# Optimization experiments

Hardware: AMD Instinct MI355X
Metric: run time of the kernel (lower is better)

Reference implementation:

```python
import jax, jax.numpy as jnp
import numpy as np

TEMPERATURE = 0.07
IGNORE_INDEX = 255
MAX_SAMPLES = 1024  # K
BACKGROUND = 0
EPS = 1e-8


def setup_inputs() -> dict:
    key = jax.random.key(0)
    k1, k2 = jax.random.split(key)
    B, C, H, W = 16, 256, 128, 128
    feats = jax.random.normal(k1, (B, C, H, W), dtype=jnp.float32)
    labels = jax.random.randint(k2, (B, H, W), 0, 4).astype(jnp.int64)
    return {"feats": feats, "labels": labels}


def _sample_pixels(feats_flat, labels_flat, K):
    """Deterministic analogue of the torch sampler: positives first, then
    background negatives, invalid last (original uses randperm; the math
    downstream is identical for any such selection). Pads exactly like the
    original: zero features, ignore_index labels, boolean valid mask."""
    # priority: 0 = foreground pos, 1 = background neg, 2 = ignore
    prio = jnp.where(labels_flat == IGNORE_INDEX, 2,
                     jnp.where(labels_flat == BACKGROUND, 1, 0))
    order = jnp.argsort(prio, axis=1)[:, :K]                      # [B, K] stable sort
    sel_prio = jnp.take_along_axis(prio, order, axis=1)
    valid = sel_prio < 2                                          # [B, K] bool
    s_feats = jnp.take_along_axis(feats_flat, order[:, :, None], axis=1)
    s_feats = s_feats * valid[:, :, None].astype(s_feats.dtype)   # zero-pad like F.pad
    s_labels = jnp.where(valid, jnp.take_along_axis(labels_flat, order, axis=1),
                         IGNORE_INDEX)
    return s_feats, s_labels, valid


def reference(feats, labels):
    B, C, H, W = feats.shape
    K = MAX_SAMPLES
    f = feats.transpose(0, 2, 3, 1).reshape(B, H * W, C)          # [B, N, C]
    l = labels.reshape(B, H * W)

    s_feats, s_labels, valid = _sample_pixels(f, l, K)

    # pair each image with the next (rolled) image -> [B, 2K, .]
    fp = jnp.concatenate([s_feats, jnp.roll(s_feats, -1, axis=0)], axis=1)
    lp = jnp.concatenate([s_labels, jnp.roll(s_labels, -1, axis=0)], axis=1)
    vp = jnp.concatenate([valid, jnp.roll(valid, -1, axis=0)], axis=1)

    # F.normalize(dim=2), eps=1e-12
    fp = fp / jnp.maximum(jnp.linalg.norm(fp, axis=2, keepdims=True), 1e-12)

    vf = vp.astype(fp.dtype)
    logits = jnp.einsum('bkc,bjc->bkj', fp, fp) / TEMPERATURE      # [B, 2K, 2K]
    logits = logits - jax.lax.stop_gradient(jnp.max(logits, axis=2, keepdims=True))

    v_matrix = vf[:, :, None] * vf[:, None, :]
    pos_mask = (lp[:, :, None] == lp[:, None, :]).astype(fp.dtype) * v_matrix
    same_img = jnp.kron(jnp.eye(2, dtype=fp.dtype), jnp.ones((K, K), dtype=fp.dtype))[None]
    neg_mask = (1.0 - pos_mask) * same_img * v_matrix
    not_self = 1.0 - jnp.eye(2 * K, dtype=fp.dtype)[None]
    pos_mask = pos_mask * not_self
    neg_mask = neg_mask * not_self

    exp_logits = jnp.exp(logits)
    sum_neg = jnp.sum(exp_logits * neg_mask, axis=2, keepdims=True)
    log_probs = logits - jnp.log(exp_logits + sum_neg + EPS)

    num_pos = jnp.maximum(pos_mask.sum(axis=2), 1.0)
    mean_log_prob = (pos_mask * log_probs).sum(axis=2) / num_pos
    valid_anchors = (pos_mask.sum(axis=2) > 0).astype(fp.dtype)
    loss_img = (-mean_log_prob * valid_anchors).sum(axis=1) / jnp.maximum(
        valid_anchors.sum(axis=1), 1.0)                            # [B]

    # with valid labels everywhere, every chunk is valid -> divide by B
    return loss_img.sum() / B
```

## Files before the change

### kernel.cpp

```cpp
#include <hip/hip_runtime.h>
#include <hip/hip_bf16.h>

namespace {

constexpr int NB  = 16;
constexpr int NC  = 256;
constexpr int NHW = 16384;
constexpr int NK  = 1024;
constexpr int IGN = 255;
constexpr float SCALE = 4.5398164f;
constexpr float CBIAS = 20.609929f;
constexpr float LN2   = 0.69314718f;

typedef __attribute__((ext_vector_type(8))) short short8;
typedef __attribute__((ext_vector_type(4))) float f32x4;
typedef unsigned int u32;

#define ASM_VMCNT8 asm volatile("s_waitcnt vmcnt(8)" ::: "memory")
#define ASM_VMCNT0 asm volatile("s_waitcnt vmcnt(0)" ::: "memory")
#define ASM_LGKM0  asm volatile("s_waitcnt lgkmcnt(0)" ::: "memory")
#define SCHEDB     __builtin_amdgcn_sched_barrier(0)
#define MEMFENCE   asm volatile("" ::: "memory")
#define BARRIER    __builtin_amdgcn_s_barrier()

__device__ __forceinline__ float fexp2(float x) {
#if __has_builtin(__builtin_amdgcn_exp2f)
  return __builtin_amdgcn_exp2f(x);
#else
  return exp2f(x);
#endif
}

__device__ __forceinline__ void gl_lds16(const void* g, void* l) {
  __builtin_amdgcn_global_load_lds((const __attribute__((address_space(1))) u32*)g,
                                   (__attribute__((address_space(3))) u32*)l, 16, 0, 0);
}

__global__ __launch_bounds__(256) void pcl_sample(const int* __restrict__ labels,
                                                  int* __restrict__ sel_lab,
                                                  int* __restrict__ sel_idx,
                                                  int* __restrict__ counter) {
  const int b = blockIdx.x, t = threadIdx.x, lane = t & 63, w = t >> 6;
  if (b == 0 && t == 0) counter[0] = 0;
  __shared__ int labL[NHW];
  __shared__ int wtot[4];

  for (int k = t; k < NK; k += 256) {
    sel_lab[b * NK + k] = IGN;
    sel_idx[b * NK + k] = 0;
  }

  const int* lab = labels + b * NHW;
  for (int k = 0; k < 64; ++k) {
    int idx = k * 256 + t;
    int pos = (idx & ~63) | ((idx & 63) ^ ((idx >> 6) & 31));
    labL[pos] = lab[idx];
  }
  __syncthreads();

  const int base = t * 64, m5 = t & 31;
  int cfg = 0, cbg = 0;
  for (int i = 0; i < 64; ++i) {
    int L = labL[base + (i ^ m5)];
    cfg += (L != IGN && L != 0);
    cbg += (L == 0);
  }
  int packed = cfg | (cbg << 15);
  int incl = packed;
#pragma unroll
  for (int off = 1; off < 64; off <<= 1) {
    int n = __shfl_up(incl, off);
    if (lane >= off) incl += n;
  }
  if (lane == 63) wtot[w] = incl;
  __syncthreads();
  int wb = 0, total = 0;
  for (int ww = 0; ww < 4; ++ww) { int v = wtot[ww]; total += v; if (ww < w) wb += v; }
  int excl = incl - packed + wb;
  int rf  = excl & 32767;
  int rbg = (excl >> 15) & 32767;
  const int nfg = total & 32767;
  if (rf < NK || nfg + rbg < NK) {
    for (int i = 0; i < 64; ++i) {
      int L = labL[base + (i ^ m5)];
      if (L == IGN) continue;
      if (L != 0) {
        if (rf < NK) { sel_lab[b * NK + rf] = L; sel_idx[b * NK + rf] = base + i; }
        ++rf;
      } else {
        int s = nfg + rbg;
        if (s < NK) { sel_lab[b * NK + s] = L; sel_idx[b * NK + s] = base + i; }
        ++rbg;
      }
    }
  }
}

__global__ __launch_bounds__(1024) void pcl_gather(const float* __restrict__ feats,
                                                   const int* __restrict__ sel_lab,
                                                   const int* __restrict__ sel_idx,
                                                   unsigned short* __restrict__ SF) {
  const int b = blockIdx.x >> 4, kb = blockIdx.x & 15;
  const int t = threadIdx.x, s = t & 63, w = t >> 6;
  __shared__ float fbuf[64][257];
  __shared__ float sqs[16][64];
  __shared__ float rn[64];
  const int gk = b * NK + kb * 64 + s;
  const int lb = sel_lab[gk];
  const int p = (lb != IGN) ? sel_idx[gk] : -1;
  const float* fb = feats + (size_t)b * NC * NHW;
  float sq = 0.f;
#pragma unroll
  for (int cc = 0; cc < 16; ++cc) {
    int c = w * 16 + cc;
    float v = (p >= 0) ? fb[(size_t)c * NHW + p] : 0.f;
    fbuf[s][c] = v;
    sq += v * v;
  }
  sqs[w][s] = sq;
  __syncthreads();
  if (t < 64) {
    float tot = 0.f;
#pragma unroll
    for (int k2 = 0; k2 < 16; ++k2) tot += sqs[k2][t];
    rn[t] = SCALE / fmaxf(sqrtf(tot), 1e-12f);
  }
  __syncthreads();
#pragma unroll
  for (int it = 0; it < 2; ++it) {
    int slot = it * 1024 + t;
    int ss = slot >> 5, ch = slot & 31;
    float r = rn[ss];
    short8 v8;
#pragma unroll
    for (int e = 0; e < 8; ++e) {
      float x = fbuf[ss][ch * 8 + e] * r;
      __hip_bfloat16 h = __float2bfloat16(x);
      unsigned short u; __builtin_memcpy(&u, &h, 2);
      v8[e] = (short)u;
    }
    *(short8*)(SF + ((size_t)(b * NK + kb * 64 + ss)) * NC + ch * 8) = v8;
  }
}

__global__ __launch_bounds__(512) void pcl_tiles(
    const unsigned short* __restrict__ SF, const int* __restrict__ sel_lab,
    float2* __restrict__ SNd, float4* __restrict__ Rii, float4* __restrict__ Rin,
    float4* __restrict__ Cp) {
  const int id = blockIdx.x;
  const int i = id & 15, strip = id >> 4, inxt = (i + 1) & 15;
  const int t = threadIdx.x, lane = t & 63, w = t >> 6;
  const int rw = w & 3, ch2 = w >> 2;
  const int lg = lane >> 4, lr = lane & 15;

  __shared__ short buf[2][128 * 256];
  __shared__ float4 colAcc[4][128];
  __shared__ float4 rred[2][64];

  const unsigned short* SFrow = SF + (size_t)i * (NK * NC) + strip * 64 * NC;

  auto stage_round = [&](int rr) {
    const unsigned short* base =
        SF + (size_t)((rr < 8) ? i : inxt) * (NK * NC) + ((rr & 7) * 128) * NC;
    short* dst = buf[rr & 1];
#pragma unroll
    for (int it = 0; it < 8; ++it) {
      int n = it * 512 + t, row = n >> 5, ch = n & 31;
      gl_lds16(base + row * NC + ((ch ^ (row & 15)) << 3), dst + (size_t)n * 8);
    }
  };

#pragma unroll
  for (int it = 0; it < 4; ++it) {
    int n = it * 512 + t, row = n >> 5, ch = n & 31;
    gl_lds16(SFrow + row * NC + ((ch ^ (row & 15)) << 3), buf[0] + (size_t)n * 8);
  }
  ASM_VMCNT0; MEMFENCE; BARRIER; MEMFENCE;

  short8 afrag[8];
  const int arow = rw * 16 + lr;
#pragma unroll
  for (int ks = 0; ks < 8; ++ks) {
    int ch = ks * 4 + lg;
    afrag[ks] = *(const short8*)(buf[0] + arow * 256 + ((ch ^ (arow & 15)) << 3));
  }
  ASM_LGKM0; SCHEDB; MEMFENCE; BARRIER; MEMFENCE;

  stage_round(0);
  stage_round(1);

  int rlab[4];
#pragma unroll
  for (int jj = 0; jj < 4; ++jj) {
    int L = sel_lab[i * NK + strip * 64 + rw * 16 + 4 * lg + jj];
    rlab[jj] = (L == IGN) ? -1 : L;
  }

  ASM_VMCNT8; MEMFENCE; BARRIER; MEMFENCE;

  float S1[4], NP[4], PE[4], SNL[4];
#pragma unroll
  for (int jj = 0; jj < 4; ++jj) { S1[jj] = 0.f; NP[jj] = 0.f; PE[jj] = 0.f; SNL[jj] = 0.f; }

  for (int r = 0; r < 8; ++r) {
    int cl[4];
#pragma unroll
    for (int c2 = 0; c2 < 4; ++c2)
      cl[c2] = sel_lab[i * NK + r * 128 + ch2 * 64 + c2 * 16 + lr];

    const short* bbase = buf[r & 1];
    f32x4 acc[4];
#pragma unroll
    for (int c2 = 0; c2 < 4; ++c2) acc[c2] = f32x4{0.f, 0.f, 0.f, 0.f};
#pragma unroll
    for (int ks = 0; ks < 8; ++ks) {
      int ch = ks * 4 + lg;
      short8 af = afrag[ks];
#pragma unroll
      for (int c2 = 0; c2 < 4; ++c2) {
        int brow = ch2 * 64 + c2 * 16 + lr;
        short8 bf = *(const short8*)(bbase + brow * 256 + ((ch ^ (brow & 15)) << 3));
        acc[c2] = __builtin_amdgcn_mfma_f32_16x16x32_bf16(af, bf, acc[c2], 0, 0, 0);
      }
    }

    const int grb = strip * 64 + rw * 16 + 4 * lg;
#pragma unroll
    for (int c2 = 0; c2 < 4; ++c2) {
      const bool cv = (cl[c2] != IGN);
      const int gc = r * 128 + ch2 * 64 + c2 * 16 + lr;
#pragma unroll
      for (int jj = 0; jj < 4; ++jj) {
        float y = acc[c2][jj] - CBIAS;
        float E = fexp2(y);
        bool pos = cv && (rlab[jj] == cl[c2]) && (grb + jj != gc);
        bool neg = cv && (rlab[jj] != cl[c2]);
        float pm = pos ? 1.f : 0.f;
        S1[jj] += pm * y; NP[jj] += pm; PE[jj] += pm * E;
        SNL[jj] += neg ? E : 0.f;
      }
    }

    MEMFENCE; BARRIER; MEMFENCE;
    stage_round(r + 2);
    ASM_VMCNT8;
    MEMFENCE; BARRIER; MEMFENCE;
  }

#pragma unroll
  for (int jj = 0; jj < 4; ++jj) {
    float a = S1[jj], b4 = NP[jj], c4 = PE[jj], d4 = SNL[jj];
#pragma unroll
    for (int m = 1; m <= 8; m <<= 1) {
      a += __shfl_xor(a, m); b4 += __shfl_xor(b4, m);
      c4 += __shfl_xor(c4, m); d4 += __shfl_xor(d4, m);
    }
    if (lr == 4 * lg + jj) rred[ch2][rw * 16 + 4 * lg + jj] = make_float4(a, b4, c4, d4);
  }
  ASM_LGKM0; SCHEDB; MEMFENCE; BARRIER; MEMFENCE;
  if (ch2 == 0) {
#pragma unroll
    for (int jj = 0; jj < 4; ++jj) {
      if (lr == 4 * lg + jj) {
        int row = rw * 16 + 4 * lg + jj;
        float4 A4 = rred[0][row], B4 = rred[1][row];
        float sn = A4.w + B4.w + 1e-8f;
        int g = i * NK + strip * 64 + row;
        SNd[g] = make_float2(__logf(sn), 1.f / sn);
        Rii[g] = make_float4(A4.x + B4.x, A4.y + B4.y, A4.z + B4.z, 0.f);
      }
    }
  }
#pragma unroll
  for (int jj = 0; jj < 4; ++jj) { S1[jj] = 0.f; NP[jj] = 0.f; PE[jj] = 0.f; }

  for (int r = 8; r < 16; ++r) {
    int cl[4];
#pragma unroll
    for (int c2 = 0; c2 < 4; ++c2)
      cl[c2] = sel_lab[inxt * NK + (r & 7) * 128 + ch2 * 64 + c2 * 16 + lr];

    const short* bbase = buf[r & 1];
    f32x4 acc[4];
#pragma unroll
    for (int c2 = 0; c2 < 4; ++c2) acc[c2] = f32x4{0.f, 0.f, 0.f, 0.f};
#pragma unroll
    for (int ks = 0; ks < 8; ++ks) {
      int ch = ks * 4 + lg;
      short8 af = afrag[ks];
#pragma unroll
      for (int c2 = 0; c2 < 4; ++c2) {
        int brow = ch2 * 64 + c2 * 16 + lr;
        short8 bf = *(const short8*)(bbase + brow * 256 + ((ch ^ (brow & 15)) << 3));
        acc[c2] = __builtin_amdgcn_mfma_f32_16x16x32_bf16(af, bf, acc[c2], 0, 0, 0);
      }
    }

#pragma unroll
    for (int c2 = 0; c2 < 4; ++c2) {
      const bool cv = (cl[c2] != IGN);
      float cS = 0.f, cN = 0.f, cE = 0.f;
#pragma unroll
      for (int jj = 0; jj < 4; ++jj) {
        float y = acc[c2][jj] - CBIAS;
        float E = fexp2(y);
        float pm = (cv && (rlab[jj] == cl[c2])) ? 1.f : 0.f;
        S1[jj] += pm * y; NP[jj] += pm; PE[jj] += pm * E;
        cS += pm * y; cN += pm; cE += pm * E;
      }
      cS += __shfl_xor(cS, 16); cS += __shfl_xor(cS, 32);
      cN += __shfl_xor(cN, 16); cN += __shfl_xor(cN, 32);
      cE += __shfl_xor(cE, 16); cE += __shfl_xor(cE, 32);
      if (lg == 0) colAcc[rw][ch2 * 64 + c2 * 16 + lr] = make_float4(cS, cN, cE, 0.f);
    }
    ASM_LGKM0; SCHEDB;
    MEMFENCE; BARRIER; MEMFENCE;
    if (rw == 0) {
      int col = ch2 * 64 + lane;
      float4 A4 = colAcc[0][col], B4 = colAcc[1][col];
      float4 C4 = colAcc[2][col], D4 = colAcc[3][col];
      Cp[(i * 16 + strip) * NK + (r & 7) * 128 + col] =
          make_float4(A4.x + B4.x + C4.x + D4.x, A4.y + B4.y + C4.y + D4.y,
                      A4.z + B4.z + C4.z + D4.z, 0.f);
    }
    if (r < 14) { stage_round(r + 2); ASM_VMCNT8; }
    else if (r == 14) { ASM_VMCNT0; }
    if (r < 15) { MEMFENCE; BARRIER; MEMFENCE; }
  }

#pragma unroll
  for (int jj = 0; jj < 4; ++jj) {
    float a = S1[jj], b4 = NP[jj], c4 = PE[jj];
#pragma unroll
    for (int m = 1; m <= 8; m <<= 1) {
      a += __shfl_xor(a, m); b4 += __shfl_xor(b4, m); c4 += __shfl_xor(c4, m);
    }
    if (lr == 4 * lg + jj) rred[ch2][rw * 16 + 4 * lg + jj] = make_float4(a, b4, c4, 0.f);
  }
  ASM_LGKM0; SCHEDB; MEMFENCE; BARRIER; MEMFENCE;
  if (ch2 == 0) {
#pragma unroll
    for (int jj = 0; jj < 4; ++jj) {
      if (lr == 4 * lg + jj) {
        int row = rw * 16 + 4 * lg + jj;
        float4 A4 = rred[0][row], B4 = rred[1][row];
        Rin[i * NK + strip * 64 + row] =
            make_float4(A4.x + B4.x, A4.y + B4.y, A4.z + B4.z, 0.f);
      }
    }
  }
}

__global__ __launch_bounds__(1024) void pcl_assemble(const float4* __restrict__ Rii,
                                                     const float4* __restrict__ Rin,
                                                     const float4* __restrict__ Cp,
                                                     const float2* __restrict__ SNd,
                                                     float* __restrict__ Aimg,
                                                     int* __restrict__ counter,
                                                     float* __restrict__ out) {
  const int i = blockIdx.x, t = threadIdx.x, lane = t & 63, w = t >> 6;
  const int prev = (i + 15) & 15;
  const int r = t;
  float a1n = 0.f, a1c = 0.f, a2n = 0.f, a2c = 0.f;
  {
    float4 rii = Rii[i * NK + r];
    float4 rin = Rin[i * NK + r];
    float2 sn = SNd[i * NK + r];
    float pp_ii = LN2 * rii.x - rii.y * sn.x - sn.y * rii.z;
    float pp_in = LN2 * rin.x - rin.y * sn.x - sn.y * rin.z;
    float np1 = rii.y + rin.y;
    if (np1 > 0.f) { a1n = -(pp_ii + pp_in) / np1; a1c = 1.f; }
    float cs1 = 0.f, cnp = 0.f, cpe = 0.f;
#pragma unroll
    for (int s2 = 0; s2 < 16; ++s2) {
      float4 c = Cp[(prev * 16 + s2) * NK + r];
      cs1 += c.x; cnp += c.y; cpe += c.z;
    }
    float ppc = LN2 * cs1 - cnp * sn.x - sn.y * cpe;
    float np2 = rii.y + cnp;
    if (np2 > 0.f) { a2n = -(pp_ii + ppc) / np2; a2c = 1.f; }
  }
#pragma unroll
  for (int m = 1; m <= 32; m <<= 1) {
    a1n += __shfl_xor(a1n, m); a1c += __shfl_xor(a1c, m);
    a2n += __shfl_xor(a2n, m); a2c += __shfl_xor(a2c, m);
  }
  __shared__ float wred[16][4];
  __shared__ int lastf;
  if (lane == 0) { wred[w][0] = a1n; wred[w][1] = a1c; wred[w][2] = a2n; wred[w][3] = a2c; }
  __syncthreads();
  if (t == 0) {
    float s0 = 0.f, s1 = 0.f, s2 = 0.f, s3 = 0.f;
#pragma unroll
    for (int k2 = 0; k2 < 16; ++k2) {
      s0 += wred[k2][0]; s1 += wred[k2][1]; s2 += wred[k2][2]; s3 += wred[k2][3];
    }
    Aimg[i * 4 + 0] = s0; Aimg[i * 4 + 1] = s1;
    Aimg[i * 4 + 2] = s2; Aimg[i * 4 + 3] = s3;
    __threadfence();
    int old = atomicAdd(counter, 1);
    lastf = (old == NB - 1);
  }
  __syncthreads();
  if (lastf && t < 64) {
    float v = 0.f;
    if (t < NB) {
      int nb = (t + 1) & 15;
      float num = __hip_atomic_load(&Aimg[t * 4 + 0], __ATOMIC_ACQUIRE, __HIP_MEMORY_SCOPE_AGENT)
                + __hip_atomic_load(&Aimg[nb * 4 + 2], __ATOMIC_ACQUIRE, __HIP_MEMORY_SCOPE_AGENT);
      float cnt = __hip_atomic_load(&Aimg[t * 4 + 1], __ATOMIC_ACQUIRE, __HIP_MEMORY_SCOPE_AGENT)
                + __hip_atomic_load(&Aimg[nb * 4 + 3], __ATOMIC_ACQUIRE, __HIP_MEMORY_SCOPE_AGENT);
      v = num / fmaxf(cnt, 1.f);
    }
    v += __shfl_xor(v, 1); v += __shfl_xor(v, 2); v += __shfl_xor(v, 4); v += __shfl_xor(v, 8);
    if (t == 0) out[0] = v / (float)NB;
  }
}

}

extern "C" void kernel_launch(void* const* d_in, const int* in_sizes, int n_in,
                              void* d_out, int out_size, void* d_ws, size_t ws_size,
                              hipStream_t stream) {
  (void)in_sizes; (void)n_in; (void)out_size; (void)ws_size;
  const float* feats  = (const float*)d_in[0];
  const int*   labels = (const int*)d_in[1];
  float* out = (float*)d_out;
  char* ws = (char*)d_ws;

  int* sel_lab = (int*)ws;
  int* sel_idx = (int*)(ws + (64 << 10));
  unsigned short* SF = (unsigned short*)(ws + (128 << 10));
  size_t off = (128 << 10) + (size_t)NB * NK * NC * 2;
  float2* SNd = (float2*)(ws + off);  off += (size_t)NB * NK * 8;
  float4* Rii = (float4*)(ws + off);  off += (size_t)NB * NK * 16;
  float4* Rin = (float4*)(ws + off);  off += (size_t)NB * NK * 16;
  float4* Cp  = (float4*)(ws + off);  off += (size_t)NB * 16 * NK * 16;
  float* Aimg = (float*)(ws + off);   off += 64 * sizeof(float);
  int* counter = (int*)(ws + off);

  pcl_sample<<<NB, 256, 0, stream>>>(labels, sel_lab, sel_idx, counter);
  pcl_gather<<<256, 1024, 0, stream>>>(feats, sel_lab, sel_idx, SF);
  pcl_tiles<<<256, 512, 0, stream>>>(SF, sel_lab, SNd, Rii, Rin, Cp);
  pcl_assemble<<<NB, 1024, 0, stream>>>(Rii, Rin, Cp, SNd, Aimg, counter, out);
}
```

Baseline: 92.40 us.

## Fuse assemble stage into tiles kernel and retile MFMA to 2x2 per wave

The final assembly kernel is folded into the tiles kernel. Per-image atomic counters let the last finishing block of each image pair do the cross-strip reduction and write the final loss, which removes one launch and the Rin buffer. Each wave now computes a 2x2 grid of 16x16 MFMA tiles, so A and B fragments are reused. The bias subtraction is moved out of the exp loop and applied algebraically afterwards via a scale factor. The sampling kernel moves to 1024 threads with a padded LDS layout. The cost is a serialized tail in the last blocks and more registers per wave.

Measured after the change: 87.61 us. 5.2% less time.

```diff
diff --git a/kernel.cpp b/kernel.cpp
--- a/kernel.cpp
+++ b/kernel.cpp
@@ -22,46 +22,39 @@
 #define SCHEDB     __builtin_amdgcn_sched_barrier(0)
 #define MEMFENCE   asm volatile("" ::: "memory")
 #define BARRIER    __builtin_amdgcn_s_barrier()
-
-__device__ __forceinline__ float fexp2(float x) {
-#if __has_builtin(__builtin_amdgcn_exp2f)
-  return __builtin_amdgcn_exp2f(x);
-#else
-  return exp2f(x);
-#endif
-}
+#define ACQ_AGENT  __builtin_amdgcn_fence(__ATOMIC_ACQUIRE, "agent")
+
+__device__ __forceinline__ float fexp2(float x) { return __builtin_exp2f(x); }
 
 __device__ __forceinline__ void gl_lds16(const void* g, void* l) {
   __builtin_amdgcn_global_load_lds((const __attribute__((address_space(1))) u32*)g,
                                    (__attribute__((address_space(3))) u32*)l, 16, 0, 0);
 }
 
-__global__ __launch_bounds__(256) void pcl_sample(const int* __restrict__ labels,
-                                                  int* __restrict__ sel_lab,
-                                                  int* __restrict__ sel_idx,
-                                                  int* __restrict__ counter) {
+__global__ __launch_bounds__(1024) void pcl_sample(const int* __restrict__ labels,
+                                                   int* __restrict__ sel_lab,
+                                                   int* __restrict__ sel_idx,
+                                                   int* __restrict__ cnt,
+                                                   int* __restrict__ findone) {
   const int b = blockIdx.x, t = threadIdx.x, lane = t & 63, w = t >> 6;
-  if (b == 0 && t == 0) counter[0] = 0;
-  __shared__ int labL[NHW];
-  __shared__ int wtot[4];
-
-  for (int k = t; k < NK; k += 256) {
-    sel_lab[b * NK + k] = IGN;
-    sel_idx[b * NK + k] = 0;
-  }
+  if (t == 0) { cnt[b] = 0; if (b == 0) *findone = 0; }
+  __shared__ int labL[1024 * 17];
+  __shared__ int wtot[16];
+
+  sel_lab[b * NK + t] = IGN;
 
   const int* lab = labels + b * NHW;
-  for (int k = 0; k < 64; ++k) {
-    int idx = k * 256 + t;
-    int pos = (idx & ~63) | ((idx & 63) ^ ((idx >> 6) & 31));
-    labL[pos] = lab[idx];
-  }
-  __syncthreads();
-
-  const int base = t * 64, m5 = t & 31;
+#pragma unroll
+  for (int k = 0; k < 16; ++k) {
+    int idx = k * 1024 + t;
+    labL[(idx >> 4) * 17 + (idx & 15)] = lab[idx];
+  }
+  __syncthreads();
+
   int cfg = 0, cbg = 0;
-  for (int i = 0; i < 64; ++i) {
-    int L = labL[base + (i ^ m5)];
+#pragma unroll
+  for (int i = 0; i < 16; ++i) {
+    int L = labL[t * 17 + i];
     cfg += (L != IGN && L != 0);
     cbg += (L == 0);
   }
@@ -75,21 +68,23 @@
   if (lane == 63) wtot[w] = incl;
   __syncthreads();
   int wb = 0, total = 0;
-  for (int ww = 0; ww < 4; ++ww) { int v = wtot[ww]; total += v; if (ww < w) wb += v; }
+#pragma unroll
+  for (int ww = 0; ww < 16; ++ww) { int v = wtot[ww]; total += v; if (ww < w) wb += v; }
   int excl = incl - packed + wb;
   int rf  = excl & 32767;
   int rbg = (excl >> 15) & 32767;
   const int nfg = total & 32767;
   if (rf < NK || nfg + rbg < NK) {
-    for (int i = 0; i < 64; ++i) {
-      int L = labL[base + (i ^ m5)];
+#pragma unroll
+    for (int i = 0; i < 16; ++i) {
+      int L = labL[t * 17 + i];
       if (L == IGN) continue;
       if (L != 0) {
-        if (rf < NK) { sel_lab[b * NK + rf] = L; sel_idx[b * NK + rf] = base + i; }
+        if (rf < NK) { sel_lab[b * NK + rf] = L; sel_idx[b * NK + rf] = t * 16 + i; }
         ++rf;
       } else {
         int s = nfg + rbg;
-        if (s < NK) { sel_lab[b * NK + s] = L; sel_idx[b * NK + s] = base + i; }
+        if (s < NK) { sel_lab[b * NK + s] = L; sel_idx[b * NK + s] = t * 16 + i; }
         ++rbg;
       }
     }
@@ -145,17 +140,23 @@
 
 __global__ __launch_bounds__(512) void pcl_tiles(
     const unsigned short* __restrict__ SF, const int* __restrict__ sel_lab,
-    float2* __restrict__ SNd, float4* __restrict__ Rii, float4* __restrict__ Rin,
-    float4* __restrict__ Cp) {
+    float2* __restrict__ SNd, float4* __restrict__ Rii, float4* __restrict__ Cp,
+    float2* __restrict__ A1arr, float2* __restrict__ Aimg,
+    int* __restrict__ cnt, int* __restrict__ findone, float* __restrict__ out) {
   const int id = blockIdx.x;
-  const int i = id & 15, strip = id >> 4, inxt = (i + 1) & 15;
+  const int i = id & 15, strip = id >> 4;
+  const int inxt = (i + 1) & 15, iprev = (i + 15) & 15;
   const int t = threadIdx.x, lane = t & 63, w = t >> 6;
-  const int rw = w & 3, ch2 = w >> 2;
+  const int rw = w & 1, ch4 = w >> 1;
   const int lg = lane >> 4, lr = lane & 15;
+  const float SFAC = __builtin_exp2f(-CBIAS);
 
   __shared__ short buf[2][128 * 256];
-  __shared__ float4 colAcc[4][128];
-  __shared__ float4 rred[2][64];
+  __shared__ float4 colAcc[2][128];
+  __shared__ float4 rredS[4][64];
+  __shared__ float4 rredX[4][64];
+  __shared__ float2 fold2[8];
+  __shared__ int fA, fB;
 
   const unsigned short* SFrow = SF + (size_t)i * (NK * NC) + strip * 64 * NC;
 
@@ -177,69 +178,94 @@
   }
   ASM_VMCNT0; MEMFENCE; BARRIER; MEMFENCE;
 
-  short8 afrag[8];
-  const int arow = rw * 16 + lr;
-#pragma unroll
-  for (int ks = 0; ks < 8; ++ks) {
-    int ch = ks * 4 + lg;
-    afrag[ks] = *(const short8*)(buf[0] + arow * 256 + ((ch ^ (arow & 15)) << 3));
+  short8 afrag[2][8];
+#pragma unroll
+  for (int rt = 0; rt < 2; ++rt) {
+    const int arow = rw * 32 + rt * 16 + lr;
+#pragma unroll
+    for (int ks = 0; ks < 8; ++ks) {
+      int ch = ks * 4 + lg;
+      afrag[rt][ks] = *(const short8*)(buf[0] + arow * 256 + ((ch ^ (arow & 15)) << 3));
+    }
   }
   ASM_LGKM0; SCHEDB; MEMFENCE; BARRIER; MEMFENCE;
 
   stage_round(0);
   stage_round(1);
 
-  int rlab[4];
-#pragma unroll
-  for (int jj = 0; jj < 4; ++jj) {
-    int L = sel_lab[i * NK + strip * 64 + rw * 16 + 4 * lg + jj];
-    rlab[jj] = (L == IGN) ? -1 : L;
-  }
+  int rlab[2][4];
+#pragma unroll
+  for (int rt = 0; rt < 2; ++rt)
+#pragma unroll
+    for (int jj = 0; jj < 4; ++jj) {
+      int L = sel_lab[i * NK + strip * 64 + rw * 32 + rt * 16 + 4 * lg + jj];
+      rlab[rt][jj] = (L == IGN) ? -1 : L;
+    }
 
   ASM_VMCNT8; MEMFENCE; BARRIER; MEMFENCE;
 
-  float S1[4], NP[4], PE[4], SNL[4];
-#pragma unroll
-  for (int jj = 0; jj < 4; ++jj) { S1[jj] = 0.f; NP[jj] = 0.f; PE[jj] = 0.f; SNL[jj] = 0.f; }
+  float SA[2][4], NPr[2][4], PEr[2][4], ETr[2][4];
+#pragma unroll
+  for (int rt = 0; rt < 2; ++rt)
+#pragma unroll
+    for (int jj = 0; jj < 4; ++jj) { SA[rt][jj] = 0.f; NPr[rt][jj] = 0.f; PEr[rt][jj] = 0.f; ETr[rt][jj] = 0.f; }
+
+  const int rs = strip >> 1;
+  const bool dwave = ((ch4 >> 1) == (strip & 1));
 
   for (int r = 0; r < 8; ++r) {
-    int cl[4];
-#pragma unroll
-    for (int c2 = 0; c2 < 4; ++c2)
-      cl[c2] = sel_lab[i * NK + r * 128 + ch2 * 64 + c2 * 16 + lr];
-
-    const short* bbase = buf[r & 1];
-    f32x4 acc[4];
-#pragma unroll
-    for (int c2 = 0; c2 < 4; ++c2) acc[c2] = f32x4{0.f, 0.f, 0.f, 0.f};
+    int cl[2]; float cvf[2];
+#pragma unroll
+    for (int c2 = 0; c2 < 2; ++c2) {
+      int L = sel_lab[i * NK + r * 128 + ch4 * 32 + c2 * 16 + lr];
+      cl[c2] = (L == IGN) ? -2 : L;
+      cvf[c2] = (L == IGN) ? 0.f : 1.f;
+    }
+
+    const short* bb = buf[r & 1];
+    f32x4 acc[2][2];
+#pragma unroll
+    for (int rt = 0; rt < 2; ++rt)
+#pragma unroll
+      for (int c2 = 0; c2 < 2; ++c2) acc[rt][c2] = f32x4{0.f, 0.f, 0.f, 0.f};
 #pragma unroll
     for (int ks = 0; ks < 8; ++ks) {
       int ch = ks * 4 + lg;
-      short8 af = afrag[ks];
-#pragma unroll
-      for (int c2 = 0; c2 < 4; ++c2) {
-        int brow = ch2 * 64 + c2 * 16 + lr;
-        short8 bf = *(const short8*)(bbase + brow * 256 + ((ch ^ (brow & 15)) << 3));
-        acc[c2] = __builtin_amdgcn_mfma_f32_16x16x32_bf16(af, bf, acc[c2], 0, 0, 0);
-      }
-    }
-
-    const int grb = strip * 64 + rw * 16 + 4 * lg;
-#pragma unroll
-    for (int c2 = 0; c2 < 4; ++c2) {
-      const bool cv = (cl[c2] != IGN);
-      const int gc = r * 128 + ch2 * 64 + c2 * 16 + lr;
-#pragma unroll
-      for (int jj = 0; jj < 4; ++jj) {
-        float y = acc[c2][jj] - CBIAS;
-        float E = fexp2(y);
-        bool pos = cv && (rlab[jj] == cl[c2]) && (grb + jj != gc);
-        bool neg = cv && (rlab[jj] != cl[c2]);
-        float pm = pos ? 1.f : 0.f;
-        S1[jj] += pm * y; NP[jj] += pm; PE[jj] += pm * E;
-        SNL[jj] += neg ? E : 0.f;
-      }
-    }
+      short8 b0, b1;
+      {
+        int br0 = ch4 * 32 + lr, br1 = ch4 * 32 + 16 + lr;
+        b0 = *(const short8*)(bb + br0 * 256 + ((ch ^ (br0 & 15)) << 3));
+        b1 = *(const short8*)(bb + br1 * 256 + ((ch ^ (br1 & 15)) << 3));
+      }
+      acc[0][0] = __builtin_amdgcn_mfma_f32_16x16x32_bf16(afrag[0][ks], b0, acc[0][0], 0, 0, 0);
+      acc[0][1] = __builtin_amdgcn_mfma_f32_16x16x32_bf16(afrag[0][ks], b1, acc[0][1], 0, 0, 0);
+      acc[1][0] = __builtin_amdgcn_mfma_f32_16x16x32_bf16(afrag[1][ks], b0, acc[1][0], 0, 0, 0);
+      acc[1][1] = __builtin_amdgcn_mfma_f32_16x16x32_bf16(afrag[1][ks], b1, acc[1][1], 0, 0, 0);
+    }
+
+    const bool isdiag = (r == rs) && dwave;
+#pragma unroll
+    for (int rt = 0; rt < 2; ++rt)
+#pragma unroll
+      for (int c2 = 0; c2 < 2; ++c2) {
+        const int clc = cl[c2]; const float cvc = cvf[c2];
+        const int gc = r * 128 + ch4 * 32 + c2 * 16 + lr;
+        const int grb = strip * 64 + rw * 32 + rt * 16 + 4 * lg;
+#pragma unroll
+        for (int jj = 0; jj < 4; ++jj) {
+          float a = acc[rt][c2][jj];
+          float E = fexp2(a);
+          float Ev = cvc * E;
+          float pm = (rlab[rt][jj] == clc) ? 1.f : 0.f;
+          if (isdiag) {
+            bool ok = (grb + jj) != gc;
+            pm = ok ? pm : 0.f;
+            Ev = ok ? Ev : 0.f;
+          }
+          SA[rt][jj] += pm * a; NPr[rt][jj] += pm;
+          PEr[rt][jj] += pm * Ev; ETr[rt][jj] += Ev;
+        }
+      }
 
     MEMFENCE; BARRIER; MEMFENCE;
     stage_round(r + 2);
@@ -248,173 +274,190 @@
   }
 
 #pragma unroll
-  for (int jj = 0; jj < 4; ++jj) {
-    float a = S1[jj], b4 = NP[jj], c4 = PE[jj], d4 = SNL[jj];
-#pragma unroll
-    for (int m = 1; m <= 8; m <<= 1) {
-      a += __shfl_xor(a, m); b4 += __shfl_xor(b4, m);
-      c4 += __shfl_xor(c4, m); d4 += __shfl_xor(d4, m);
-    }
-    if (lr == 4 * lg + jj) rred[ch2][rw * 16 + 4 * lg + jj] = make_float4(a, b4, c4, d4);
-  }
-  ASM_LGKM0; SCHEDB; MEMFENCE; BARRIER; MEMFENCE;
-  if (ch2 == 0) {
+  for (int rt = 0; rt < 2; ++rt)
 #pragma unroll
     for (int jj = 0; jj < 4; ++jj) {
-      if (lr == 4 * lg + jj) {
-        int row = rw * 16 + 4 * lg + jj;
-        float4 A4 = rred[0][row], B4 = rred[1][row];
-        float sn = A4.w + B4.w + 1e-8f;
-        int g = i * NK + strip * 64 + row;
-        SNd[g] = make_float2(__logf(sn), 1.f / sn);
-        Rii[g] = make_float4(A4.x + B4.x, A4.y + B4.y, A4.z + B4.z, 0.f);
-      }
-    }
-  }
-#pragma unroll
-  for (int jj = 0; jj < 4; ++jj) { S1[jj] = 0.f; NP[jj] = 0.f; PE[jj] = 0.f; }
+      float a = SA[rt][jj], b4 = NPr[rt][jj], c4 = PEr[rt][jj], d4 = ETr[rt][jj];
+#pragma unroll
+      for (int m = 1; m <= 8; m <<= 1) {
+        a += __shfl_xor(a, m); b4 += __shfl_xor(b4, m);
+        c4 += __shfl_xor(c4, m); d4 += __shfl_xor(d4, m);
+      }
+      if (lr == 0) rredS[ch4][rw * 32 + rt * 16 + 4 * lg + jj] = make_float4(a, b4, c4, d4);
+    }
+
+  float SX[2][4], NX[2][4], PX[2][4];
+#pragma unroll
+  for (int rt = 0; rt < 2; ++rt)
+#pragma unroll
+    for (int jj = 0; jj < 4; ++jj) { SX[rt][jj] = 0.f; NX[rt][jj] = 0.f; PX[rt][jj] = 0.f; }
 
   for (int r = 8; r < 16; ++r) {
-    int cl[4];
-#pragma unroll
-    for (int c2 = 0; c2 < 4; ++c2)
-      cl[c2] = sel_lab[inxt * NK + (r & 7) * 128 + ch2 * 64 + c2 * 16 + lr];
-
-    const short* bbase = buf[r & 1];
-    f32x4 acc[4];
-#pragma unroll
-    for (int c2 = 0; c2 < 4; ++c2) acc[c2] = f32x4{0.f, 0.f, 0.f, 0.f};
+    int cl[2];
+#pragma unroll
+    for (int c2 = 0; c2 < 2; ++c2) {
+      int L = sel_lab[inxt * NK + (r & 7) * 128 + ch4 * 32 + c2 * 16 + lr];
+      cl[c2] = (L == IGN) ? -2 : L;
+    }
+
+    const short* bb = buf[r & 1];
+    f32x4 acc[2][2];
+#pragma unroll
+    for (int rt = 0; rt < 2; ++rt)
+#pragma unroll
+      for (int c2 = 0; c2 < 2; ++c2) acc[rt][c2] = f32x4{0.f, 0.f, 0.f, 0.f};
 #pragma unroll
     for (int ks = 0; ks < 8; ++ks) {
       int ch = ks * 4 + lg;
-      short8 af = afrag[ks];
-#pragma unroll
-      for (int c2 = 0; c2 < 4; ++c2) {
-        int brow = ch2 * 64 + c2 * 16 + lr;
-        short8 bf = *(const short8*)(bbase + brow * 256 + ((ch ^ (brow & 15)) << 3));
-        acc[c2] = __builtin_amdgcn_mfma_f32_16x16x32_bf16(af, bf, acc[c2], 0, 0, 0);
-      }
-    }
-
-#pragma unroll
-    for (int c2 = 0; c2 < 4; ++c2) {
-      const bool cv = (cl[c2] != IGN);
-      float cS = 0.f, cN = 0.f, cE = 0.f;
-#pragma unroll
-      for (int jj = 0; jj < 4; ++jj) {
-        float y = acc[c2][jj] - CBIAS;
-        float E = fexp2(y);
-        float pm = (cv && (rlab[jj] == cl[c2])) ? 1.f : 0.f;
-        S1[jj] += pm * y; NP[jj] += pm; PE[jj] += pm * E;
-        cS += pm * y; cN += pm; cE += pm * E;
-      }
-      cS += __shfl_xor(cS, 16); cS += __shfl_xor(cS, 32);
-      cN += __shfl_xor(cN, 16); cN += __shfl_xor(cN, 32);
-      cE += __shfl_xor(cE, 16); cE += __shfl_xor(cE, 32);
-      if (lg == 0) colAcc[rw][ch2 * 64 + c2 * 16 + lr] = make_float4(cS, cN, cE, 0.f);
+      short8 b0, b1;
+      {
+        int br0 = ch4 * 32 + lr, br1 = ch4 * 32 + 16 + lr;
+        b0 = *(const short8*)(bb + br0 * 256 + ((ch ^ (br0 & 15)) << 3));
+        b1 = *(const short8*)(bb + br1 * 256 + ((ch ^ (br1 & 15)) << 3));
+      }
+      acc[0][0] = __builtin_amdgcn_mfma_f32_16x16x32_bf16(afrag[0][ks], b0, acc[0][0], 0, 0, 0);
+      acc[0][1] = __builtin_amdgcn_mfma_f32_16x16x32_bf16(afrag[0][ks], b1, acc[0][1], 0, 0, 0);
+      acc[1][0] = __builtin_amdgcn_mfma_f32_16x16x32_bf16(afrag[1][ks], b0, acc[1][0], 0, 0, 0);
+      acc[1][1] = __builtin_amdgcn_mfma_f32_16x16x32_bf16(afrag[1][ks], b1, acc[1][1], 0, 0, 0);
+    }
+
+    float cS[2], cN[2], cE[2];
+#pragma unroll
+    for (int c2 = 0; c2 < 2; ++c2) { cS[c2] = 0.f; cN[c2] = 0.f; cE[c2] = 0.f; }
+#pragma unroll
+    for (int rt = 0; rt < 2; ++rt)
+#pragma unroll
+      for (int c2 = 0; c2 < 2; ++c2) {
+        const int clc = cl[c2];
+#pragma unroll
+        for (int jj = 0; jj < 4; ++jj) {
+          float a = acc[rt][c2][jj];
+          float E = fexp2(a);
+          float pm = (rlab[rt][jj] == clc) ? 1.f : 0.f;
+          float pa = pm * a, pe = pm * E;
+          SX[rt][jj] += pa; NX[rt][jj] += pm; PX[rt][jj] += pe;
+          cS[c2] += pa; cN[c2] += pm; cE[c2] += pe;
+        }
+      }
+#pragma unroll
+    for (int c2 = 0; c2 < 2; ++c2) {
+      cS[c2] += __shfl_xor(cS[c2], 16); cS[c2] += __shfl_xor(cS[c2], 32);
+      cN[c2] += __shfl_xor(cN[c2], 16); cN[c2] += __shfl_xor(cN[c2], 32);
+      cE[c2] += __shfl_xor(cE[c2], 16); cE[c2] += __shfl_xor(cE[c2], 32);
+      if (lg == 0) colAcc[rw][ch4 * 32 + c2 * 16 + lr] = make_float4(cS[c2], cN[c2], cE[c2], 0.f);
     }
     ASM_LGKM0; SCHEDB;
     MEMFENCE; BARRIER; MEMFENCE;
-    if (rw == 0) {
-      int col = ch2 * 64 + lane;
-      float4 A4 = colAcc[0][col], B4 = colAcc[1][col];
-      float4 C4 = colAcc[2][col], D4 = colAcc[3][col];
-      Cp[(i * 16 + strip) * NK + (r & 7) * 128 + col] =
-          make_float4(A4.x + B4.x + C4.x + D4.x, A4.y + B4.y + C4.y + D4.y,
-                      A4.z + B4.z + C4.z + D4.z, 0.f);
-    }
-    if (r < 14) { stage_round(r + 2); ASM_VMCNT8; }
-    else if (r == 14) { ASM_VMCNT0; }
-    if (r < 15) { MEMFENCE; BARRIER; MEMFENCE; }
-  }
-
-#pragma unroll
-  for (int jj = 0; jj < 4; ++jj) {
-    float a = S1[jj], b4 = NP[jj], c4 = PE[jj];
-#pragma unroll
-    for (int m = 1; m <= 8; m <<= 1) {
-      a += __shfl_xor(a, m); b4 += __shfl_xor(b4, m); c4 += __shfl_xor(c4, m);
-    }
-    if (lr == 4 * lg + jj) rred[ch2][rw * 16 + 4 * lg + jj] = make_float4(a, b4, c4, 0.f);
-  }
-  ASM_LGKM0; SCHEDB; MEMFENCE; BARRIER; MEMFENCE;
-  if (ch2 == 0) {
+    if (rw == 1 && lg == 0) {
+#pragma unroll
+      for (int c2 = 0; c2 < 2; ++c2) {
+        int col = ch4 * 32 + c2 * 16 + lr;
+        float4 o = colAcc[0][col];
+        Cp[(i * 16 + strip) * NK + (r & 7) * 128 + col] =
+            make_float4(cS[c2] + o.x, cN[c2] + o.y, (cE[c2] + o.z) * SFAC, 0.f);
+      }
+    }
+    if (r < 14) { stage_round(r + 2); ASM_VMCNT8; MEMFENCE; BARRIER; MEMFENCE; }
+    else if (r == 14) { ASM_VMCNT0; MEMFENCE; BARRIER; MEMFENCE; }
+  }
+
+#pragma unroll
+  for (int rt = 0; rt < 2; ++rt)
 #pragma unroll
     for (int jj = 0; jj < 4; ++jj) {
-      if (lr == 4 * lg + jj) {
-        int row = rw * 16 + 4 * lg + jj;
-        float4 A4 = rred[0][row], B4 = rred[1][row];
-        Rin[i * NK + strip * 64 + row] =
-            make_float4(A4.x + B4.x, A4.y + B4.y, A4.z + B4.z, 0.f);
-      }
-    }
-  }
-}
-
-__global__ __launch_bounds__(1024) void pcl_assemble(const float4* __restrict__ Rii,
-                                                     const float4* __restrict__ Rin,
-                                                     const float4* __restrict__ Cp,
-                                                     const float2* __restrict__ SNd,
-                                                     float* __restrict__ Aimg,
-                                                     int* __restrict__ counter,
-                                                     float* __restrict__ out) {
-  const int i = blockIdx.x, t = threadIdx.x, lane = t & 63, w = t >> 6;
-  const int prev = (i + 15) & 15;
-  const int r = t;
-  float a1n = 0.f, a1c = 0.f, a2n = 0.f, a2c = 0.f;
-  {
-    float4 rii = Rii[i * NK + r];
-    float4 rin = Rin[i * NK + r];
-    float2 sn = SNd[i * NK + r];
-    float pp_ii = LN2 * rii.x - rii.y * sn.x - sn.y * rii.z;
-    float pp_in = LN2 * rin.x - rin.y * sn.x - sn.y * rin.z;
-    float np1 = rii.y + rin.y;
-    if (np1 > 0.f) { a1n = -(pp_ii + pp_in) / np1; a1c = 1.f; }
-    float cs1 = 0.f, cnp = 0.f, cpe = 0.f;
-#pragma unroll
-    for (int s2 = 0; s2 < 16; ++s2) {
-      float4 c = Cp[(prev * 16 + s2) * NK + r];
-      cs1 += c.x; cnp += c.y; cpe += c.z;
-    }
-    float ppc = LN2 * cs1 - cnp * sn.x - sn.y * cpe;
-    float np2 = rii.y + cnp;
-    if (np2 > 0.f) { a2n = -(pp_ii + ppc) / np2; a2c = 1.f; }
-  }
-#pragma unroll
-  for (int m = 1; m <= 32; m <<= 1) {
-    a1n += __shfl_xor(a1n, m); a1c += __shfl_xor(a1c, m);
-    a2n += __shfl_xor(a2n, m); a2c += __shfl_xor(a2c, m);
-  }
-  __shared__ float wred[16][4];
-  __shared__ int lastf;
-  if (lane == 0) { wred[w][0] = a1n; wred[w][1] = a1c; wred[w][2] = a2n; wred[w][3] = a2c; }
-  __syncthreads();
+      float a = SX[rt][jj], b4 = NX[rt][jj], c4 = PX[rt][jj];
+#pragma unroll
+      for (int m = 1; m <= 8; m <<= 1) {
+        a += __shfl_xor(a, m); b4 += __shfl_xor(b4, m); c4 += __shfl_xor(c4, m);
+      }
+      if (lr == 0) rredX[ch4][rw * 32 + rt * 16 + 4 * lg + jj] = make_float4(a, b4, c4, 0.f);
+    }
+  __syncthreads();
+
+  if (t < 64) {
+    float4 sS = rredS[0][t], sX = rredX[0][t];
+#pragma unroll
+    for (int c4 = 1; c4 < 4; ++c4) {
+      float4 u = rredS[c4][t], v = rredX[c4][t];
+      sS.x += u.x; sS.y += u.y; sS.z += u.z; sS.w += u.w;
+      sX.x += v.x; sX.y += v.y; sX.z += v.z;
+    }
+    float SNL = sS.w - sS.z;
+    float SN = SNL * SFAC + 1e-8f;
+    float LSN = __logf(SN), rSN = 1.f / SN;
+    int g = i * NK + strip * 64 + t;
+    SNd[g] = make_float2(LSN, rSN);
+    Rii[g] = make_float4(sS.x, sS.y, sS.z * SFAC, 0.f);
+    float pps = LN2 * (sS.x - CBIAS * sS.y) - sS.y * LSN - rSN * (sS.z * SFAC);
+    float ppx = LN2 * (sX.x - CBIAS * sX.y) - sX.y * LSN - rSN * (sX.z * SFAC);
+    float np1 = sS.y + sX.y;
+    float an = 0.f, ac = 0.f;
+    if (np1 > 0.f) { an = -(pps + ppx) / np1; ac = 1.f; }
+#pragma unroll
+    for (int m = 1; m <= 32; m <<= 1) { an += __shfl_xor(an, m); ac += __shfl_xor(ac, m); }
+    if (t == 0) A1arr[i * 16 + strip] = make_float2(an, ac);
+  }
+  __syncthreads();
+
   if (t == 0) {
-    float s0 = 0.f, s1 = 0.f, s2 = 0.f, s3 = 0.f;
-#pragma unroll
-    for (int k2 = 0; k2 < 16; ++k2) {
-      s0 += wred[k2][0]; s1 += wred[k2][1]; s2 += wred[k2][2]; s3 += wred[k2][3];
-    }
-    Aimg[i * 4 + 0] = s0; Aimg[i * 4 + 1] = s1;
-    Aimg[i * 4 + 2] = s2; Aimg[i * 4 + 3] = s3;
     __threadfence();
-    int old = atomicAdd(counter, 1);
-    lastf = (old == NB - 1);
-  }
-  __syncthreads();
-  if (lastf && t < 64) {
-    float v = 0.f;
-    if (t < NB) {
-      int nb = (t + 1) & 15;
-      float num = __hip_atomic_load(&Aimg[t * 4 + 0], __ATOMIC_ACQUIRE, __HIP_MEMORY_SCOPE_AGENT)
-                + __hip_atomic_load(&Aimg[nb * 4 + 2], __ATOMIC_ACQUIRE, __HIP_MEMORY_SCOPE_AGENT);
-      float cnt = __hip_atomic_load(&Aimg[t * 4 + 1], __ATOMIC_ACQUIRE, __HIP_MEMORY_SCOPE_AGENT)
-                + __hip_atomic_load(&Aimg[nb * 4 + 3], __ATOMIC_ACQUIRE, __HIP_MEMORY_SCOPE_AGENT);
-      v = num / fmaxf(cnt, 1.f);
-    }
-    v += __shfl_xor(v, 1); v += __shfl_xor(v, 2); v += __shfl_xor(v, 4); v += __shfl_xor(v, 8);
-    if (t == 0) out[0] = v / (float)NB;
-  }
+    int o1 = atomicAdd(&cnt[i], 1);
+    int o2 = atomicAdd(&cnt[iprev], 1);
+    fA = (o1 == 31); fB = (o2 == 31);
+  }
+  __syncthreads();
+
+  auto pair_fold = [&](int p) {
+    const int q = (p + 1) & 15;
+    ACQ_AGENT;
+    float an = 0.f, ac = 0.f;
+    for (int r2 = t; r2 < NK; r2 += 512) {
+      float4 rii = Rii[q * NK + r2];
+      float2 sn = SNd[q * NK + r2];
+      float cs = 0.f, cn = 0.f, ce = 0.f;
+#pragma unroll
+      for (int s2 = 0; s2 < 16; ++s2) {
+        float4 c = Cp[(p * 16 + s2) * NK + r2];
+        cs += c.x; cn += c.y; ce += c.z;
+      }
+      float ppc = LN2 * (cs - CBIAS * cn) - cn * sn.x - sn.y * ce;
+      float ppi = LN2 * (rii.x - CBIAS * rii.y) - rii.y * sn.x - sn.y * rii.z;
+      float np2 = rii.y + cn;
+      if (np2 > 0.f) { an -= (ppi + ppc) / np2; ac += 1.f; }
+    }
+#pragma unroll
+    for (int m = 1; m <= 32; m <<= 1) { an += __shfl_xor(an, m); ac += __shfl_xor(ac, m); }
+    if (lane == 0) fold2[w] = make_float2(an, ac);
+    __syncthreads();
+    if (t == 0) {
+      float a2n = 0.f, a2c = 0.f;
+#pragma unroll
+      for (int k2 = 0; k2 < 8; ++k2) { a2n += fold2[k2].x; a2c += fold2[k2].y; }
+      float a1n = 0.f, a1c = 0.f;
+#pragma unroll
+      for (int s2 = 0; s2 < 16; ++s2) {
+        float2 a = A1arr[q * 16 + s2];
+        a1n += a.x; a1c += a.y;
+      }
+      Aimg[q] = make_float2(a1n + a2n, a1c + a2c);
+      __threadfence();
+      int f = atomicAdd(findone, 1);
+      if (f == NB - 1) {
+        ACQ_AGENT;
+        float v = 0.f;
+#pragma unroll
+        for (int im = 0; im < NB; ++im) {
+          float2 gg = Aimg[im];
+          v += gg.x / fmaxf(gg.y, 1.f);
+        }
+        out[0] = v / (float)NB;
+      }
+    }
+    __syncthreads();
+  };
+
+  if (fA) pair_fold(i);
+  if (fB) pair_fold(iprev);
 }
 
 }
@@ -434,13 +477,14 @@
   size_t off = (128 << 10) + (size_t)NB * NK * NC * 2;
   float2* SNd = (float2*)(ws + off);  off += (size_t)NB * NK * 8;
   float4* Rii = (float4*)(ws + off);  off += (size_t)NB * NK * 16;
-  float4* Rin = (float4*)(ws + off);  off += (size_t)NB * NK * 16;
   float4* Cp  = (float4*)(ws + off);  off += (size_t)NB * 16 * NK * 16;
-  float* Aimg = (float*)(ws + off);   off += 64 * sizeof(float);
-  int* counter = (int*)(ws + off);
-
-  pcl_sample<<<NB, 256, 0, stream>>>(labels, sel_lab, sel_idx, counter);
+  float2* A1arr = (float2*)(ws + off); off += (size_t)NB * 16 * 8;
+  float2* Aimg = (float2*)(ws + off);  off += NB * 8;
+  int* cnt = (int*)(ws + off);         off += 16 * 4;
+  int* findone = (int*)(ws + off);
+
+  pcl_sample<<<NB, 1024, 0, stream>>>(labels, sel_lab, sel_idx, cnt, findone);
   pcl_gather<<<256, 1024, 0, stream>>>(feats, sel_lab, sel_idx, SF);
-  pcl_tiles<<<256, 512, 0, stream>>>(SF, sel_lab, SNd, Rii, Rin, Cp);
-  pcl_assemble<<<NB, 1024, 0, stream>>>(Rii, Rin, Cp, SNd, Aimg, counter, out);
-}
+  pcl_tiles<<<256, 512, 0, stream>>>(SF, sel_lab, SNd, Rii, Cp, A1arr, Aimg,
+                                     cnt, findone, out);
+}
```
